# Optimization experiments

Hardware: AMD Instinct MI355X
Metric: run time of the kernel (lower is better)

Reference implementation:

```python
import jax, jax.numpy as jnp
import numpy as np

HIDDEN = 768
NUM_BLOCKS = 8
BLOCK = HIDDEN // NUM_BLOCKS  # 96
FACTOR = 1
LAMBDA = 0.01  # sparsity_threshold
HTF = 1.0      # hard_thresholding_fraction
SCALE = 0.02


def setup_inputs() -> dict:
    key = jax.random.key(0)
    kx, k1, k2, k3, k4 = jax.random.split(key, 5)
    B, H, W = 2, 256, 256
    x = jax.random.normal(kx, (B, HIDDEN, H, W), dtype=jnp.float32)
    w1 = SCALE * jax.random.normal(k1, (NUM_BLOCKS, BLOCK, BLOCK * FACTOR, 2), dtype=jnp.float32)
    b1 = SCALE * jax.random.normal(k2, (NUM_BLOCKS, BLOCK * FACTOR, 1, 1, 2), dtype=jnp.float32)
    w2 = SCALE * jax.random.normal(k3, (NUM_BLOCKS, BLOCK * FACTOR, BLOCK, 2), dtype=jnp.float32)
    b2 = SCALE * jax.random.normal(k4, (NUM_BLOCKS, BLOCK, 1, 1, 2), dtype=jnp.float32)
    return {"x": x, "w1": w1, "b1": b1, "w2": w2, "b2": b2}


def _compl_mul_add(a, w, c):
    # a: (b,k,i,x,y,2) real/imag pairs; w: (k,i,o,2); c: (k,o,1,1,2)
    ar, ai = a[..., 0], a[..., 1]
    wr, wi = w[..., 0], w[..., 1]
    rr = jnp.einsum('bkixy,kio->bkoxy', ar, wr)
    ii = jnp.einsum('bkixy,kio->bkoxy', ai, wi)
    ir = jnp.einsum('bkixy,kio->bkoxy', ai, wr)
    ri = jnp.einsum('bkixy,kio->bkoxy', ar, wi)
    return jnp.stack([rr - ii, ir + ri], axis=-1) + c


def _softshrink(x, lam):
    return jnp.where(x > lam, x - lam, jnp.where(x < -lam, x + lam, jnp.zeros_like(x)))


def reference(x, w1, b1, w2, b2):
    B, C, H, W = x.shape
    total_modes = H // 2 + 1
    kept = int(total_modes * HTF)
    bias = x
    xf = jnp.fft.rfft2(x, s=(H, W), axes=(-2, -1), norm='ortho')  # (B,C,H,W//2+1)
    xf = xf.reshape(B, NUM_BLOCKS, BLOCK, H, W // 2 + 1)
    xr = jnp.stack([jnp.real(xf), jnp.imag(xf)], axis=-1)  # view_as_real
    lo, hi = total_modes - kept, total_modes + kept
    o1 = jax.nn.relu(_compl_mul_add(xr[:, :, :, lo:hi, :kept, :], w1, b1))
    o2 = jnp.zeros_like(xr).at[:, :, :, lo:hi, :kept, :].set(_compl_mul_add(o1, w2, b2))
    s = _softshrink(o2, LAMBDA)
    xc = (s[..., 0] + 1j * s[..., 1]).reshape(B, C, H, W // 2 + 1)
    out = jnp.fft.irfft2(xc, s=(H, W), axes=(-2, -1), norm='ortho').astype(x.dtype)
    return out + bias
```

## Files before the change

### kernel.cpp

```cpp
#include <hip/hip_runtime.h>
#include <hip/hip_bf16.h>
#include <math.h>


#define LAMBDA_SS 0.01f

typedef unsigned int u32;
typedef __attribute__((ext_vector_type(8))) short bf16x8;
typedef __attribute__((ext_vector_type(4))) float f32x4;

__device__ __forceinline__ u32 pack_bf16(float r, float i) {
  union { float f; u32 u; } ur, ui;
  ur.f = r; ui.f = i;
  u32 rb = (ur.u + 0x7FFFu + ((ur.u >> 16) & 1u)) >> 16;
  u32 ib = (ui.u + 0x7FFFu + ((ui.u >> 16) & 1u)) >> 16;
  return (ib << 16) | (rb & 0xFFFFu);
}

__device__ __forceinline__ float2 unpack_bf16(u32 p) {
  union { u32 u; float f; } a, b;
  a.u = (p & 0xFFFFu) << 16;
  b.u = (p & 0xFFFF0000u);
  return make_float2(a.f, b.f);
}

__device__ __forceinline__ float sshrink(float v) {
  return (v > LAMBDA_SS) ? v - LAMBDA_SS : ((v < -LAMBDA_SS) ? v + LAMBDA_SS : 0.f);
}

__device__ __forceinline__ float2 cadd(float2 a, float2 b){ return make_float2(a.x+b.x, a.y+b.y); }
__device__ __forceinline__ float2 csub(float2 a, float2 b){ return make_float2(a.x-b.x, a.y-b.y); }
__device__ __forceinline__ float2 cmul(float2 a, float2 b){
  return make_float2(fmaf(a.x,b.x,-a.y*b.y), fmaf(a.x,b.y,a.y*b.x));
}
__device__ __forceinline__ float2 cmulj(float2 a, float si){
  return make_float2(-si*a.y, si*a.x);
}
__device__ __forceinline__ float2 shflx(float2 v, int m){
  return make_float2(__shfl_xor(v.x, m, 64), __shfl_xor(v.y, m, 64));
}
__device__ __forceinline__ float2 shfll(float2 v, int l){
  return make_float2(__shfl(v.x, l, 64), __shfl(v.y, l, 64));
}
__device__ __forceinline__ int brev6(int x){ return (int)(__brev((u32)x) >> 26); }

struct Tw { float2 t128, t64, t32, t16, t8, t4; float si; };

__device__ __forceinline__ float2 mkTw(int e, float si){
  float a = (float)e * 0.0245436926f;
  return make_float2(cosf(a), si*sinf(a));
}
__device__ __forceinline__ Tw make_tw(int lane, float si){
  Tw w; w.si = si;
  w.t128 = mkTw(lane, si);
  w.t64  = mkTw(2*lane, si);
  w.t32  = mkTw((lane&31)*4, si);
  w.t16  = mkTw((lane&15)*8, si);
  w.t8   = mkTw((lane&7)*16, si);
  w.t4   = mkTw((lane&3)*32, si);
  return w;
}

__device__ __forceinline__ float2 bfly_dif(float2 v, int h, float2 th, int lane){
  float2 p = shflx(v, h);
  float sx = (lane & h) ? -1.f : 1.f;
  float2 s = make_float2(fmaf(sx, v.x, p.x), fmaf(sx, v.y, p.y));
  if (lane & h) s = cmul(s, th);
  return s;
}
__device__ __forceinline__ float2 bfly_dit(float2 v, int h, float2 th, int lane){
  if (lane & h) v = cmul(v, th);
  float2 p = shflx(v, h);
  float sx = (lane & h) ? -1.f : 1.f;
  return make_float2(fmaf(sx, v.x, p.x), fmaf(sx, v.y, p.y));
}

__device__ __forceinline__ void fft256_dif(float2 v[4], int lane, const Tw& T){
  float2 t128b = cmulj(T.t128, T.si);
  { float2 a=v[0], b=v[2]; v[0]=cadd(a,b); v[2]=cmul(csub(a,b), T.t128);
    float2 c=v[1], d=v[3]; v[1]=cadd(c,d); v[3]=cmul(csub(c,d), t128b); }
  { float2 a=v[0], b=v[1]; v[0]=cadd(a,b); v[1]=cmul(csub(a,b), T.t64);
    float2 c=v[2], d=v[3]; v[2]=cadd(c,d); v[3]=cmul(csub(c,d), T.t64); }
#pragma unroll
  for (int r=0;r<4;++r) v[r]=bfly_dif(v[r],32,T.t32,lane);
#pragma unroll
  for (int r=0;r<4;++r) v[r]=bfly_dif(v[r],16,T.t16,lane);
#pragma unroll
  for (int r=0;r<4;++r) v[r]=bfly_dif(v[r],8,T.t8,lane);
#pragma unroll
  for (int r=0;r<4;++r) v[r]=bfly_dif(v[r],4,T.t4,lane);
#pragma unroll
  for (int r=0;r<4;++r){
    float2 p=shflx(v[r],2);
    float sx=(lane&2)?-1.f:1.f;
    float2 s=make_float2(fmaf(sx,v[r].x,p.x), fmaf(sx,v[r].y,p.y));
    if ((lane&3)==3) s=cmulj(s,T.si);
    v[r]=s;
  }
#pragma unroll
  for (int r=0;r<4;++r){
    float2 p=shflx(v[r],1);
    float sx=(lane&1)?-1.f:1.f;
    v[r]=make_float2(fmaf(sx,v[r].x,p.x), fmaf(sx,v[r].y,p.y));
  }
}

__device__ __forceinline__ void fft256_dit(float2 v[4], int lane, const Tw& T){
#pragma unroll
  for (int r=0;r<4;++r){
    float2 p=shflx(v[r],1);
    float sx=(lane&1)?-1.f:1.f;
    v[r]=make_float2(fmaf(sx,v[r].x,p.x), fmaf(sx,v[r].y,p.y));
  }
#pragma unroll
  for (int r=0;r<4;++r){
    float2 w=v[r];
    if ((lane&3)==3) w=cmulj(w,T.si);
    float2 p=shflx(w,2);
    float sx=(lane&2)?-1.f:1.f;
    v[r]=make_float2(fmaf(sx,w.x,p.x), fmaf(sx,w.y,p.y));
  }
#pragma unroll
  for (int r=0;r<4;++r) v[r]=bfly_dit(v[r],4,T.t4,lane);
#pragma unroll
  for (int r=0;r<4;++r) v[r]=bfly_dit(v[r],8,T.t8,lane);
#pragma unroll
  for (int r=0;r<4;++r) v[r]=bfly_dit(v[r],16,T.t16,lane);
#pragma unroll
  for (int r=0;r<4;++r) v[r]=bfly_dit(v[r],32,T.t32,lane);
  { v[1]=cmul(v[1],T.t64); float2 a=v[0]; v[0]=cadd(a,v[1]); v[1]=csub(a,v[1]);
    v[3]=cmul(v[3],T.t64); float2 c=v[2]; v[2]=cadd(c,v[3]); v[3]=csub(c,v[3]); }
  { v[2]=cmul(v[2],T.t128); v[3]=cmul(v[3], cmulj(T.t128,T.si));
    float2 a=v[0]; v[0]=cadd(a,v[2]); v[2]=csub(a,v[2]);
    float2 b=v[1]; v[1]=cadd(b,v[3]); v[3]=csub(b,v[3]); }
}

__device__ __forceinline__ int stage_row(int kw){ return 33*(kw&3) + (kw>>2); }

__global__ __launch_bounds__(256) void k_rowfft(const float* __restrict__ x, u32* __restrict__ F) {
  __shared__ u32 stage[131*65];
  const int bc = blockIdx.x >> 2, hc = blockIdx.x & 3;
  const int tid = threadIdx.x, wave = tid >> 6, lane = tid & 63;
  Tw T = make_tw(lane, -1.f);
  const int L = brev6(lane);
  const int laneP0 = brev6((64 - L) & 63);
  const int lanePX = 63 - lane;

  for (int rr = 0; rr < 8; ++rr) {
    const int hl0 = wave*16 + rr*2, hl1 = hl0 + 1;
    const float* xa = x + ((size_t)bc*256 + hc*64 + hl0) * 256;
    float2 v[4];
#pragma unroll
    for (int r=0;r<4;++r){ int d = lane + 64*r; v[r] = make_float2(xa[d], xa[256+d]); }
    fft256_dif(v, lane, T);
#define UNSCR(R, RP, C, LP) { \
      float2 z = v[R]; float2 p = shfll(v[RP], LP); \
      float2 A  = make_float2(0.5f*(z.x+p.x), 0.5f*(z.y-p.y)); \
      float2 Bv = make_float2(0.5f*(z.y+p.y), 0.5f*(p.x-z.x)); \
      int kw = 4*L + (C); \
      if (kw <= 128) { int row = stage_row(kw); \
        stage[row*65 + hl0] = pack_bf16(A.x, A.y); \
        stage[row*65 + hl1] = pack_bf16(Bv.x, Bv.y); } }
    UNSCR(0, 0, 0, laneP0)
    UNSCR(1, 1, 2, lanePX)
    UNSCR(2, 3, 1, lanePX)
    UNSCR(3, 2, 3, lanePX)
#undef UNSCR
  }
  __syncthreads();
  for (int idx = tid; idx < 129*64; idx += 256) {
    int kw = idx >> 6, hl = idx & 63;
    F[((size_t)bc*129 + kw)*256 + hc*64 + hl] = stage[stage_row(kw)*65 + hl];
  }
}

__global__ __launch_bounds__(256) void k_prep_w(const float2* __restrict__ w1,
                                                const float2* __restrict__ w2,
                                                u32* __restrict__ Wt) {
  const int blk = blockIdx.x;
  const int k = blk >> 1, layer = blk & 1;
  const float2* w = (layer == 0 ? w1 : w2) + (size_t)k * 96 * 96;
  u32* out = Wt + (size_t)blk * 18432;
  for (int idx = threadIdx.x; idx < 9216; idx += 256) {
    int o = idx % 96, i = idx / 96;
    float2 v = w[i * 96 + o];
    out[(2 * o) * 96 + i]     = pack_bf16(v.x, -v.y);
    out[(2 * o + 1) * 96 + i] = pack_bf16(v.y, v.x);
  }
}

#define CM_LDS_BYTES 99072

__global__ __launch_bounds__(512, 2) void k_colmix(u32* __restrict__ F,
    const u32* __restrict__ Wt,
    const float2* __restrict__ b1, const float2* __restrict__ b2) {
  extern __shared__ char smem[];

  const int bi = (blockIdx.x & 7) * 258 + (blockIdx.x >> 3);
  const int kw = bi % 129;
  const int bk = bi / 129;
  const int k = bk & 7, b = bk >> 3;
  const int t = threadIdx.x;
  const int lane = t & 63, wave = t >> 6;
  const int wm = wave >> 2, wn = wave & 3;
  const int lrow = lane & 15;
  const int g = lane >> 4;
  const int lk = g * 16;

  const size_t chstride = 129 * 256;
  const size_t colbase = (((size_t)(b*768 + k*96)) * 129 + kw) * 256;

  {
    Tw Tf = make_tw(lane, -1.f);
    u32 raw[12][4];
#pragma unroll
    for (int cc = 0; cc < 12; ++cc) {
      const u32* p = F + colbase + (size_t)(wave*12 + cc) * chstride;
#pragma unroll
      for (int r = 0; r < 4; ++r) raw[cc][r] = p[lane + 64*r];
    }
    const float s = 1.f/256.f;
#pragma unroll
    for (int cc = 0; cc < 12; ++cc) {
      float2 v[4];
#pragma unroll
      for (int r = 0; r < 4; ++r) v[r] = unpack_bf16(raw[cc][r]);
      fft256_dif(v, lane, Tf);
      const int c = wave*12 + cc;
#pragma unroll
      for (int r = 0; r < 4; ++r) {
        int n = lane + 64*r;
        int byte = n*384 + c*4;
        *reinterpret_cast<u32*>(smem + (byte ^ ((n&7)<<4))) = pack_bf16(v[r].x*s, v[r].y*s);
      }
    }
  }
  __syncthreads();

  const bf16x8* W1v = reinterpret_cast<const bf16x8*>(Wt + (size_t)(k*2 + 0) * 18432);
  const bf16x8* W2v = reinterpret_cast<const bf16x8*>(Wt + (size_t)(k*2 + 1) * 18432);

  f32x4 acc[6][4];

#pragma unroll
  for (int mi = 0; mi < 6; ++mi)
#pragma unroll
    for (int ni = 0; ni < 4; ++ni) acc[mi][ni] = (f32x4)0.f;
  {
    bf16x8 af[2][6];
#pragma unroll
    for (int mi = 0; mi < 6; ++mi)
      af[0][mi] = W1v[(wm*96 + mi*16 + lrow)*24 + g];
#pragma unroll
    for (int ks = 0; ks < 6; ++ks) {
      if (ks < 5) {
#pragma unroll
        for (int mi = 0; mi < 6; ++mi)
          af[(ks+1)&1][mi] = W1v[(wm*96 + mi*16 + lrow)*24 + (ks+1)*4 + g];
      }
      bf16x8 bf[4];
#pragma unroll
      for (int ni = 0; ni < 4; ++ni) {
        int n = wn*64 + ni*16 + lrow;
        int byte = n*384 + ks*64 + lk;
        bf[ni] = *reinterpret_cast<bf16x8*>(smem + (byte ^ ((n&7)<<4)));
      }
#pragma unroll
      for (int ni = 0; ni < 4; ++ni)
#pragma unroll
        for (int mi = 0; mi < 6; ++mi)
          acc[mi][ni] = __builtin_amdgcn_mfma_f32_16x16x32_bf16(af[ks&1][mi], bf[ni], acc[mi][ni], 0, 0, 0);
    }
  }
  __syncthreads();

  {
    const float2* b1k = b1 + k * 96;
#pragma unroll
    for (int mi = 0; mi < 6; ++mi) {
      int m0 = wm*96 + mi*16 + 4*g;
      int o0 = m0 >> 1;
      float2 ba = b1k[o0], bb = b1k[o0 + 1];
#pragma unroll
      for (int ni = 0; ni < 4; ++ni) {
        int n = wn*64 + ni*16 + lrow;
        f32x4 v = acc[mi][ni];
        u32 lo = pack_bf16(fmaxf(v[0] + ba.x, 0.f), fmaxf(v[1] + ba.y, 0.f));
        u32 hi = pack_bf16(fmaxf(v[2] + bb.x, 0.f), fmaxf(v[3] + bb.y, 0.f));
        int byte = n*384 + m0*2;
        *reinterpret_cast<uint2*>(smem + (byte ^ ((n&7)<<4))) = make_uint2(lo, hi);
      }
    }
  }
  __syncthreads();

#pragma unroll
  for (int mi = 0; mi < 6; ++mi)
#pragma unroll
    for (int ni = 0; ni < 4; ++ni) acc[mi][ni] = (f32x4)0.f;
  {
    bf16x8 af[2][6];
#pragma unroll
    for (int mi = 0; mi < 6; ++mi)
      af[0][mi] = W2v[(wm*96 + mi*16 + lrow)*24 + g];
#pragma unroll
    for (int ks = 0; ks < 6; ++ks) {
      if (ks < 5) {
#pragma unroll
        for (int mi = 0; mi < 6; ++mi)
          af[(ks+1)&1][mi] = W2v[(wm*96 + mi*16 + lrow)*24 + (ks+1)*4 + g];
      }
      bf16x8 bf[4];
#pragma unroll
      for (int ni = 0; ni < 4; ++ni) {
        int n = wn*64 + ni*16 + lrow;
        int byte = n*384 + ks*64 + lk;
        bf[ni] = *reinterpret_cast<bf16x8*>(smem + (byte ^ ((n&7)<<4)));
      }
#pragma unroll
      for (int ni = 0; ni < 4; ++ni)
#pragma unroll
        for (int mi = 0; mi < 6; ++mi)
          acc[mi][ni] = __builtin_amdgcn_mfma_f32_16x16x32_bf16(af[ks&1][mi], bf[ni], acc[mi][ni], 0, 0, 0);
    }
  }
  __syncthreads();

  {
    u32* Clds = reinterpret_cast<u32*>(smem);
    const float2* b2k = b2 + k * 96;
#pragma unroll
    for (int mi = 0; mi < 6; ++mi) {
      int m0 = wm*96 + mi*16 + 4*g;
      int o0 = m0 >> 1;
      float2 ca = b2k[o0], cb = b2k[o0 + 1];
#pragma unroll
      for (int ni = 0; ni < 4; ++ni) {
        int n = wn*64 + ni*16 + lrow;
        f32x4 v = acc[mi][ni];
        Clds[o0*258 + n]       = pack_bf16(sshrink(v[0] + ca.x), sshrink(v[1] + ca.y));
        Clds[(o0 + 1)*258 + n] = pack_bf16(sshrink(v[2] + cb.x), sshrink(v[3] + cb.y));
      }
    }
  }
  __syncthreads();

  {
    const u32* Clds = reinterpret_cast<const u32*>(smem);
    Tw Ti = make_tw(lane, 1.f);
    const float s = 1.f/256.f;
#pragma unroll
    for (int cc = 0; cc < 12; ++cc) {
      const int c = wave*12 + cc;
      float2 v[4];
#pragma unroll
      for (int r = 0; r < 4; ++r) v[r] = unpack_bf16(Clds[c*258 + lane + 64*r]);
      fft256_dit(v, lane, Ti);
      u32* p = F + colbase + (size_t)c * chstride;
#pragma unroll
      for (int r = 0; r < 4; ++r) p[lane + 64*r] = pack_bf16(v[r].x*s, v[r].y*s);
    }
  }
}

__global__ __launch_bounds__(256) void k_rowifft(const u32* __restrict__ F,
                                                 const float* __restrict__ x,
                                                 float* __restrict__ out) {
  __shared__ u32 stage[131*65];
  const int bc = blockIdx.x >> 2, hc = blockIdx.x & 3;
  const int tid = threadIdx.x, wave = tid >> 6, lane = tid & 63;
  Tw T = make_tw(lane, 1.f);
  for (int idx = tid; idx < 129*64; idx += 256) {
    int kw = idx >> 6, hl = idx & 63;
    stage[stage_row(kw)*65 + hl] = F[((size_t)bc*129 + kw)*256 + hc*64 + hl];
  }
  __syncthreads();

  const int L = brev6(lane);
  for (int rr = 0; rr < 8; ++rr) {
    const int hl0 = wave*16 + rr*2, hl1 = hl0 + 1;
    float2 v[4];
#pragma unroll
    for (int r=0;r<4;++r) {
      int c = ((r&1)<<1) | (r>>1);
      int kw = 4*L + c;
      int src = (kw <= 128) ? kw : 256 - kw;
      float sg = (kw <= 128) ? 1.f : -1.f;
      int row = stage_row(src);
      float2 a = unpack_bf16(stage[row*65 + hl0]);
      float2 b = unpack_bf16(stage[row*65 + hl1]);
      a.y *= sg; b.y *= sg;
      if (kw == 0 || kw == 128) { a.y = 0.f; b.y = 0.f; }
      v[r] = make_float2(a.x - b.y, a.y + b.x);
    }
    fft256_dit(v, lane, T);
    const float* xa = x   + ((size_t)bc*256 + hc*64 + hl0) * 256;
    float*       oa = out + ((size_t)bc*256 + hc*64 + hl0) * 256;
#pragma unroll
    for (int r=0;r<4;++r) {
      int d = lane + 64*r;
      oa[d]       = v[r].x + xa[d];
      oa[256 + d] = v[r].y + xa[256 + d];
    }
  }
}

extern "C" void kernel_launch(void* const* d_in, const int* in_sizes, int n_in,
                              void* d_out, int out_size, void* d_ws, size_t ws_size,
                              hipStream_t stream) {
  const float* x   = (const float*)d_in[0];
  const float2* w1 = (const float2*)d_in[1];
  const float2* b1 = (const float2*)d_in[2];
  const float2* w2 = (const float2*)d_in[3];
  const float2* b2 = (const float2*)d_in[4];
  float* out = (float*)d_out;
  u32* F = (u32*)d_ws;
  u32* Wt = (u32*)d_out;

  (void)hipFuncSetAttribute(reinterpret_cast<const void*>(k_colmix),
                            hipFuncAttributeMaxDynamicSharedMemorySize, CM_LDS_BYTES);

  const int n_rows_blocks = 1536 * 4;
  const int n_cm_blocks   = 2 * 8 * 129;

  k_prep_w<<<16, 256, 0, stream>>>(w1, w2, Wt);
  k_rowfft<<<n_rows_blocks, 256, 0, stream>>>(x, F);
  k_colmix<<<n_cm_blocks, 512, CM_LDS_BYTES, stream>>>(F, Wt, b1, b2);
  k_rowifft<<<n_rows_blocks, 256, 0, stream>>>(F, x, out);
}
```

Baseline: 908.7 us.

## Double colmix threads and use contiguous-element FFT layout with vectorized loads

The column-mix kernel now runs 1024 threads per block instead of 512. Each wave does half as many channel FFTs and half as many MFMA M-tiles. The column FFTs switch to a layout with four contiguous elements per lane, using per-stage twiddles from sincosf, 16-byte global loads and stores, and a new LDS XOR swizzle. The aim is more latency hiding and fewer, wider memory transactions. The (1024,4) launch bound may force a tight register budget and cause spills, and only one block fits per CU because of the LDS footprint.

New measurement: 886.8 us. 1.02x faster.

```diff
diff --git a/kernel.cpp b/kernel.cpp
--- a/kernel.cpp
+++ b/kernel.cpp
@@ -135,7 +135,69 @@
     float2 b=v[1]; v[1]=cadd(b,v[3]); v[3]=csub(b,v[3]); }
 }
 
+__device__ __forceinline__ void make_tws4(int lane, float si, float2 tws[6][4]) {
+#pragma unroll
+  for (int r=0;r<4;++r){
+    int e = (4*lane + r) & 127;
+    float a = si * (float)e * 0.0245436926f;
+    float sn, cs;
+    sincosf(a, &sn, &cs);
+    float2 t = make_float2(cs, sn);
+    tws[0][r] = t;
+#pragma unroll
+    for (int s=1; s<6; ++s) {
+      float2 sq = cmul(t, t);
+      if (e & 64) { sq.x = -sq.x; sq.y = -sq.y; }
+      e = (2*e) & 127;
+      t = sq;
+      tws[s][r] = t;
+    }
+  }
+}
+
+__device__ __forceinline__ void fft256_dif4(float2 v[4], int lane,
+                                            const float2 tws[6][4], float si){
+#pragma unroll
+  for (int s=0;s<6;++s){
+    const int m = 32>>s;
+#pragma unroll
+    for (int r=0;r<4;++r){
+      float2 p = shflx(v[r], m);
+      float sx = (lane & m) ? -1.f : 1.f;
+      float2 t = make_float2(fmaf(sx, v[r].x, p.x), fmaf(sx, v[r].y, p.y));
+      float2 tm = cmul(t, tws[s][r]);
+      v[r] = (lane & m) ? tm : t;
+    }
+  }
+  { float2 a0=v[0], a2=v[2]; v[0]=cadd(a0,a2); v[2]=csub(a0,a2);
+    float2 a1=v[1], a3=v[3]; v[1]=cadd(a1,a3); v[3]=cmulj(csub(a1,a3), si); }
+  { float2 a=v[0]; v[0]=cadd(a,v[1]); v[1]=csub(a,v[1]);
+    float2 c=v[2]; v[2]=cadd(c,v[3]); v[3]=csub(c,v[3]); }
+}
+
+__device__ __forceinline__ void fft256_dit4(float2 v[4], int lane,
+                                            const float2 tws[6][4], float si){
+  { float2 a=v[0]; v[0]=cadd(a,v[1]); v[1]=csub(a,v[1]);
+    float2 c=v[2]; v[2]=cadd(c,v[3]); v[3]=csub(c,v[3]); }
+  { v[3] = cmulj(v[3], si);
+    float2 a0=v[0]; v[0]=cadd(a0,v[2]); v[2]=csub(a0,v[2]);
+    float2 a1=v[1]; v[1]=cadd(a1,v[3]); v[3]=csub(a1,v[3]); }
+#pragma unroll
+  for (int s=5;s>=0;--s){
+    const int m = 32>>s;
+#pragma unroll
+    for (int r=0;r<4;++r){
+      float2 wm_ = cmul(v[r], tws[s][r]);
+      float2 w = (lane & m) ? wm_ : v[r];
+      float2 p = shflx(w, m);
+      float sx = (lane & m) ? -1.f : 1.f;
+      v[r] = make_float2(fmaf(sx, w.x, p.x), fmaf(sx, w.y, p.y));
+    }
+  }
+}
+
 __device__ __forceinline__ int stage_row(int kw){ return 33*(kw&3) + (kw>>2); }
+__device__ __forceinline__ int dslot(int n){ return (((n>>2)&7) ^ ((n&3)<<1)) << 4; }
 
 __global__ __launch_bounds__(256) void k_rowfft(const float* __restrict__ x, u32* __restrict__ F) {
   __shared__ u32 stage[131*65];
@@ -191,7 +253,7 @@
 
 #define CM_LDS_BYTES 99072
 
-__global__ __launch_bounds__(512, 2) void k_colmix(u32* __restrict__ F,
+__global__ __launch_bounds__(1024, 4) void k_colmix(u32* __restrict__ F,
     const u32* __restrict__ Wt,
     const float2* __restrict__ b1, const float2* __restrict__ b2) {
   extern __shared__ char smem[];
@@ -205,33 +267,35 @@
   const int wm = wave >> 2, wn = wave & 3;
   const int lrow = lane & 15;
   const int g = lane >> 4;
-  const int lk = g * 16;
 
   const size_t chstride = 129 * 256;
   const size_t colbase = (((size_t)(b*768 + k*96)) * 129 + kw) * 256;
 
   {
-    Tw Tf = make_tw(lane, -1.f);
-    u32 raw[12][4];
-#pragma unroll
-    for (int cc = 0; cc < 12; ++cc) {
-      const u32* p = F + colbase + (size_t)(wave*12 + cc) * chstride;
-#pragma unroll
-      for (int r = 0; r < 4; ++r) raw[cc][r] = p[lane + 64*r];
-    }
+    uint4 raw[6];
+#pragma unroll
+    for (int cc = 0; cc < 6; ++cc)
+      raw[cc] = *reinterpret_cast<const uint4*>(F + colbase + (size_t)(wave*6 + cc)*chstride + 4*lane);
+
+    float2 tws[6][4];
+    make_tws4(lane, -1.f, tws);
     const float s = 1.f/256.f;
 #pragma unroll
-    for (int cc = 0; cc < 12; ++cc) {
-      float2 v[4];
-#pragma unroll
-      for (int r = 0; r < 4; ++r) v[r] = unpack_bf16(raw[cc][r]);
-      fft256_dif(v, lane, Tf);
-      const int c = wave*12 + cc;
+    for (int pp = 0; pp < 3; ++pp) {
+      float2 va[4], vb[4];
+      va[0]=unpack_bf16(raw[2*pp].x);   va[1]=unpack_bf16(raw[2*pp].y);
+      va[2]=unpack_bf16(raw[2*pp].z);   va[3]=unpack_bf16(raw[2*pp].w);
+      vb[0]=unpack_bf16(raw[2*pp+1].x); vb[1]=unpack_bf16(raw[2*pp+1].y);
+      vb[2]=unpack_bf16(raw[2*pp+1].z); vb[3]=unpack_bf16(raw[2*pp+1].w);
+      fft256_dif4(va, lane, tws, -1.f);
+      fft256_dif4(vb, lane, tws, -1.f);
+      const int c0 = wave*6 + 2*pp;
 #pragma unroll
       for (int r = 0; r < 4; ++r) {
-        int n = lane + 64*r;
-        int byte = n*384 + c*4;
-        *reinterpret_cast<u32*>(smem + (byte ^ ((n&7)<<4))) = pack_bf16(v[r].x*s, v[r].y*s);
+        int n = 4*lane + r;
+        int byte = (n*384 + c0*4) ^ dslot(n);
+        *reinterpret_cast<uint2*>(smem + byte) =
+            make_uint2(pack_bf16(va[r].x*s, va[r].y*s), pack_bf16(vb[r].x*s, vb[r].y*s));
       }
     }
   }
@@ -240,35 +304,35 @@
   const bf16x8* W1v = reinterpret_cast<const bf16x8*>(Wt + (size_t)(k*2 + 0) * 18432);
   const bf16x8* W2v = reinterpret_cast<const bf16x8*>(Wt + (size_t)(k*2 + 1) * 18432);
 
-  f32x4 acc[6][4];
-
-#pragma unroll
-  for (int mi = 0; mi < 6; ++mi)
+  f32x4 acc[3][4];
+
+#pragma unroll
+  for (int mi = 0; mi < 3; ++mi)
 #pragma unroll
     for (int ni = 0; ni < 4; ++ni) acc[mi][ni] = (f32x4)0.f;
   {
-    bf16x8 af[2][6];
-#pragma unroll
-    for (int mi = 0; mi < 6; ++mi)
-      af[0][mi] = W1v[(wm*96 + mi*16 + lrow)*24 + g];
+    bf16x8 af[2][3];
+#pragma unroll
+    for (int mi = 0; mi < 3; ++mi)
+      af[0][mi] = W1v[(wm*48 + mi*16 + lrow)*24 + g];
 #pragma unroll
     for (int ks = 0; ks < 6; ++ks) {
       if (ks < 5) {
 #pragma unroll
-        for (int mi = 0; mi < 6; ++mi)
-          af[(ks+1)&1][mi] = W1v[(wm*96 + mi*16 + lrow)*24 + (ks+1)*4 + g];
+        for (int mi = 0; mi < 3; ++mi)
+          af[(ks+1)&1][mi] = W1v[(wm*48 + mi*16 + lrow)*24 + (ks+1)*4 + g];
       }
       bf16x8 bf[4];
 #pragma unroll
       for (int ni = 0; ni < 4; ++ni) {
         int n = wn*64 + ni*16 + lrow;
-        int byte = n*384 + ks*64 + lk;
-        bf[ni] = *reinterpret_cast<bf16x8*>(smem + (byte ^ ((n&7)<<4)));
+        int byte = (n*384 + ks*64 + g*16) ^ dslot(n);
+        bf[ni] = *reinterpret_cast<bf16x8*>(smem + byte);
       }
 #pragma unroll
       for (int ni = 0; ni < 4; ++ni)
 #pragma unroll
-        for (int mi = 0; mi < 6; ++mi)
+        for (int mi = 0; mi < 3; ++mi)
           acc[mi][ni] = __builtin_amdgcn_mfma_f32_16x16x32_bf16(af[ks&1][mi], bf[ni], acc[mi][ni], 0, 0, 0);
     }
   }
@@ -277,8 +341,8 @@
   {
     const float2* b1k = b1 + k * 96;
 #pragma unroll
-    for (int mi = 0; mi < 6; ++mi) {
-      int m0 = wm*96 + mi*16 + 4*g;
+    for (int mi = 0; mi < 3; ++mi) {
+      int m0 = wm*48 + mi*16 + 4*g;
       int o0 = m0 >> 1;
       float2 ba = b1k[o0], bb = b1k[o0 + 1];
 #pragma unroll
@@ -287,40 +351,40 @@
         f32x4 v = acc[mi][ni];
         u32 lo = pack_bf16(fmaxf(v[0] + ba.x, 0.f), fmaxf(v[1] + ba.y, 0.f));
         u32 hi = pack_bf16(fmaxf(v[2] + bb.x, 0.f), fmaxf(v[3] + bb.y, 0.f));
-        int byte = n*384 + m0*2;
-        *reinterpret_cast<uint2*>(smem + (byte ^ ((n&7)<<4))) = make_uint2(lo, hi);
-      }
-    }
-  }
-  __syncthreads();
-
-#pragma unroll
-  for (int mi = 0; mi < 6; ++mi)
+        int byte = (n*384 + m0*2) ^ dslot(n);
+        *reinterpret_cast<uint2*>(smem + byte) = make_uint2(lo, hi);
+      }
+    }
+  }
+  __syncthreads();
+
+#pragma unroll
+  for (int mi = 0; mi < 3; ++mi)
 #pragma unroll
     for (int ni = 0; ni < 4; ++ni) acc[mi][ni] = (f32x4)0.f;
   {
-    bf16x8 af[2][6];
-#pragma unroll
-    for (int mi = 0; mi < 6; ++mi)
-      af[0][mi] = W2v[(wm*96 + mi*16 + lrow)*24 + g];
+    bf16x8 af[2][3];
+#pragma unroll
+    for (int mi = 0; mi < 3; ++mi)
+      af[0][mi] = W2v[(wm*48 + mi*16 + lrow)*24 + g];
 #pragma unroll
     for (int ks = 0; ks < 6; ++ks) {
       if (ks < 5) {
 #pragma unroll
-        for (int mi = 0; mi < 6; ++mi)
-          af[(ks+1)&1][mi] = W2v[(wm*96 + mi*16 + lrow)*24 + (ks+1)*4 + g];
+        for (int mi = 0; mi < 3; ++mi)
+          af[(ks+1)&1][mi] = W2v[(wm*48 + mi*16 + lrow)*24 + (ks+1)*4 + g];
       }
       bf16x8 bf[4];
 #pragma unroll
       for (int ni = 0; ni < 4; ++ni) {
         int n = wn*64 + ni*16 + lrow;
-        int byte = n*384 + ks*64 + lk;
-        bf[ni] = *reinterpret_cast<bf16x8*>(smem + (byte ^ ((n&7)<<4)));
+        int byte = (n*384 + ks*64 + g*16) ^ dslot(n);
+        bf[ni] = *reinterpret_cast<bf16x8*>(smem + byte);
       }
 #pragma unroll
       for (int ni = 0; ni < 4; ++ni)
 #pragma unroll
-        for (int mi = 0; mi < 6; ++mi)
+        for (int mi = 0; mi < 3; ++mi)
           acc[mi][ni] = __builtin_amdgcn_mfma_f32_16x16x32_bf16(af[ks&1][mi], bf[ni], acc[mi][ni], 0, 0, 0);
     }
   }
@@ -330,8 +394,8 @@
     u32* Clds = reinterpret_cast<u32*>(smem);
     const float2* b2k = b2 + k * 96;
 #pragma unroll
-    for (int mi = 0; mi < 6; ++mi) {
-      int m0 = wm*96 + mi*16 + 4*g;
+    for (int mi = 0; mi < 3; ++mi) {
+      int m0 = wm*48 + mi*16 + 4*g;
       int o0 = m0 >> 1;
       float2 ca = b2k[o0], cb = b2k[o0 + 1];
 #pragma unroll
@@ -347,18 +411,32 @@
 
   {
     const u32* Clds = reinterpret_cast<const u32*>(smem);
-    Tw Ti = make_tw(lane, 1.f);
+    float2 tws[6][4];
+    make_tws4(lane, 1.f, tws);
     const float s = 1.f/256.f;
 #pragma unroll
-    for (int cc = 0; cc < 12; ++cc) {
-      const int c = wave*12 + cc;
-      float2 v[4];
-#pragma unroll
-      for (int r = 0; r < 4; ++r) v[r] = unpack_bf16(Clds[c*258 + lane + 64*r]);
-      fft256_dit(v, lane, Ti);
-      u32* p = F + colbase + (size_t)c * chstride;
-#pragma unroll
-      for (int r = 0; r < 4; ++r) p[lane + 64*r] = pack_bf16(v[r].x*s, v[r].y*s);
+    for (int pp = 0; pp < 3; ++pp) {
+      const int c0 = wave*6 + 2*pp;
+      float2 va[4], vb[4];
+      {
+        uint2 q0 = *reinterpret_cast<const uint2*>(Clds + c0*258 + 4*lane);
+        uint2 q1 = *reinterpret_cast<const uint2*>(Clds + c0*258 + 4*lane + 2);
+        va[0]=unpack_bf16(q0.x); va[1]=unpack_bf16(q0.y);
+        va[2]=unpack_bf16(q1.x); va[3]=unpack_bf16(q1.y);
+        uint2 q2 = *reinterpret_cast<const uint2*>(Clds + (c0+1)*258 + 4*lane);
+        uint2 q3 = *reinterpret_cast<const uint2*>(Clds + (c0+1)*258 + 4*lane + 2);
+        vb[0]=unpack_bf16(q2.x); vb[1]=unpack_bf16(q2.y);
+        vb[2]=unpack_bf16(q3.x); vb[3]=unpack_bf16(q3.y);
+      }
+      fft256_dit4(va, lane, tws, 1.f);
+      fft256_dit4(vb, lane, tws, 1.f);
+      uint4 oa, ob;
+      oa.x = pack_bf16(va[0].x*s, va[0].y*s); oa.y = pack_bf16(va[1].x*s, va[1].y*s);
+      oa.z = pack_bf16(va[2].x*s, va[2].y*s); oa.w = pack_bf16(va[3].x*s, va[3].y*s);
+      ob.x = pack_bf16(vb[0].x*s, vb[0].y*s); ob.y = pack_bf16(vb[1].x*s, vb[1].y*s);
+      ob.z = pack_bf16(vb[2].x*s, vb[2].y*s); ob.w = pack_bf16(vb[3].x*s, vb[3].y*s);
+      *reinterpret_cast<uint4*>(F + colbase + (size_t)c0*chstride + 4*lane) = oa;
+      *reinterpret_cast<uint4*>(F + colbase + (size_t)(c0+1)*chstride + 4*lane) = ob;
     }
   }
 }
@@ -425,6 +503,6 @@
 
   k_prep_w<<<16, 256, 0, stream>>>(w1, w2, Wt);
   k_rowfft<<<n_rows_blocks, 256, 0, stream>>>(x, F);
-  k_colmix<<<n_cm_blocks, 512, CM_LDS_BYTES, stream>>>(F, Wt, b1, b2);
+  k_colmix<<<n_cm_blocks, 1024, CM_LDS_BYTES, stream>>>(F, Wt, b1, b2);
   k_rowifft<<<n_rows_blocks, 256, 0, stream>>>(F, x, out);
 }
```
